# Performance work log

Hardware: AMD Instinct MI355X
Metric: run time of the kernel (lower is better)

The kernel has to match this reference:

```python
import jax, jax.numpy as jnp
import numpy as np

N_NODES = 100000
N_EDGES = 1600000
IN_FEAT = 128
OUT_FEAT = 128


def setup_inputs() -> dict:
    key = jax.random.key(0)
    k1, k2, k3 = jax.random.split(key, 3)
    x = jax.random.normal(k1, (N_NODES, IN_FEAT), dtype=jnp.float32)
    W = jax.random.normal(k2, (IN_FEAT, OUT_FEAT), dtype=jnp.float32) * (1.0 / np.sqrt(IN_FEAT))
    b = jnp.zeros((OUT_FEAT,), dtype=jnp.float32)
    edge_index = jax.random.randint(k3, (2, N_EDGES), 0, N_NODES, dtype=jnp.int64)
    return {"x": x, "W": W, "b": b, "edge_index": edge_index}


def reference(x, W, b, edge_index):
    # PyG GCNConv: add self-loops, symmetric deg normalization, scatter-add.
    N = x.shape[0]
    loops = jnp.arange(N, dtype=edge_index.dtype)
    ei = jnp.concatenate([edge_index, jnp.stack([loops, loops])], axis=1)  # [2, E+N]
    row, col = ei[0], ei[1]  # source, target
    ones = jnp.ones(ei.shape[1], dtype=x.dtype)
    deg = jax.ops.segment_sum(ones, col, num_segments=N)  # in-degree incl. self-loop
    deg_inv_sqrt = jnp.where(deg > 0, jax.lax.rsqrt(deg), 0.0)
    norm = deg_inv_sqrt[row] * deg_inv_sqrt[col]  # [E+N]
    xw = x @ W  # [N, out_feat]
    msg = xw[row] * norm[:, None]  # gather + normalize
    out = jax.ops.segment_sum(msg, col, num_segments=N) + b  # scatter-add + bias
    return out
```

## Files before the change

kernel.cpp:

```cpp
#include <hip/hip_runtime.h>

#define N_NODES 100000
#define N_EDGES 1600000
#define FEAT 128
#define NBUCK 782
#define BUCK_SHIFT 7
#define BUCK_MASK 127
#define GEMM_BLOCKS 1563
#define HIST_EPB 4096
#define HIST_BLOCKS 391
#define SCAT_EPB 12800
#define SCAT_BLOCKS 125
#define WT_PITCH 136

typedef __attribute__((ext_vector_type(8))) short short8;
typedef __attribute__((ext_vector_type(4))) float f32x4;

__device__ inline unsigned short f2bf(float f) {
    unsigned u = __builtin_bit_cast(unsigned, f);
    unsigned r = (u + 0x7FFFu + ((u >> 16) & 1u)) >> 16;
    return (unsigned short)r;
}
__device__ inline float bf2f(unsigned h) {
    unsigned u = h << 16;
    return __builtin_bit_cast(float, u);
}

__global__ __launch_bounds__(256)
void k_gemm_hist(const float* __restrict__ x, const float* __restrict__ W,
                 unsigned short* __restrict__ yb,
                 const int* __restrict__ col, int* __restrict__ bcnt) {
    int bid = blockIdx.x, tid = threadIdx.x;
    if (bid >= GEMM_BLOCKS) {
        __shared__ int hist[NBUCK];
        for (int i = tid; i < NBUCK; i += 256) hist[i] = 0;
        __syncthreads();
        int e0 = (bid - GEMM_BLOCKS) * HIST_EPB;
        int n = min(HIST_EPB, N_EDGES - e0);
        for (int i = tid * 4; i < n; i += 1024) {
            if (i + 3 < n) {
                int4 c4 = *(const int4*)(col + e0 + i);
                atomicAdd(&hist[c4.x >> BUCK_SHIFT], 1);
                atomicAdd(&hist[c4.y >> BUCK_SHIFT], 1);
                atomicAdd(&hist[c4.z >> BUCK_SHIFT], 1);
                atomicAdd(&hist[c4.w >> BUCK_SHIFT], 1);
            } else {
                for (int j = i; j < n; ++j) atomicAdd(&hist[col[e0 + j] >> BUCK_SHIFT], 1);
            }
        }
        __syncthreads();
        for (int i = tid; i < NBUCK; i += 256) {
            int h = hist[i];
            if (h) atomicAdd(&bcnt[i], h);
        }
        return;
    }

    __shared__ unsigned short Ws[FEAT * WT_PITCH];
    for (int idx = tid; idx < FEAT * FEAT; idx += 256) {
        int k = idx >> 7, f = idx & 127;
        Ws[f * WT_PITCH + k] = f2bf(W[idx]);
    }
    __syncthreads();

    int lane = tid & 63;
    int m = lane & 15, quad = lane >> 4;
    int node = bid * 64 + (tid >> 6) * 16 + m;
    int ldn = node < N_NODES ? node : N_NODES - 1;
    const float* xr = x + (size_t)ldn * FEAT + quad * 8;

    f32x4 acc[8];
#pragma unroll
    for (int nt = 0; nt < 8; ++nt) acc[nt] = (f32x4){0.f, 0.f, 0.f, 0.f};

#pragma unroll
    for (int kk = 0; kk < 4; ++kk) {
        float4 xa = *(const float4*)(xr + kk * 32);
        float4 xc = *(const float4*)(xr + kk * 32 + 4);
        short8 fx;
        fx[0] = (short)f2bf(xa.x); fx[1] = (short)f2bf(xa.y);
        fx[2] = (short)f2bf(xa.z); fx[3] = (short)f2bf(xa.w);
        fx[4] = (short)f2bf(xc.x); fx[5] = (short)f2bf(xc.y);
        fx[6] = (short)f2bf(xc.z); fx[7] = (short)f2bf(xc.w);
        const unsigned short* wp = Ws + kk * 32 + quad * 8;
#pragma unroll
        for (int nt = 0; nt < 8; ++nt) {
            short8 af = *(const short8*)(wp + (nt * 16 + m) * WT_PITCH);
            acc[nt] = __builtin_amdgcn_mfma_f32_16x16x32_bf16(af, fx, acc[nt], 0, 0, 0);
        }
    }

    if (node < N_NODES) {
        unsigned* yp = (unsigned*)(yb + (size_t)node * FEAT);
#pragma unroll
        for (int nt = 0; nt < 8; ++nt) {
            uint2 pk;
            pk.x = (unsigned)f2bf(acc[nt][0]) | ((unsigned)f2bf(acc[nt][1]) << 16);
            pk.y = (unsigned)f2bf(acc[nt][2]) | ((unsigned)f2bf(acc[nt][3]) << 16);
            *(uint2*)(yp + nt * 8 + quad * 2) = pk;
        }
    }
}

__global__ __launch_bounds__(256)
void k_bscatter(const int* __restrict__ row, const int* __restrict__ col,
                const int* __restrict__ bcnt, int* __restrict__ bcur0,
                int* __restrict__ bstarts, unsigned* __restrict__ ebuf) {
    __shared__ int sb[1024];
    __shared__ int csum[256];
    __shared__ int bstartsL[NBUCK];
    __shared__ int hist[NBUCK];
    __shared__ int gbase[NBUCK];
    int tid = threadIdx.x;

    for (int i = tid; i < 1024; i += 256) sb[i] = (i < NBUCK) ? bcnt[i] : 0;
    __syncthreads();
    int v0 = sb[tid * 4], v1 = sb[tid * 4 + 1], v2 = sb[tid * 4 + 2], v3 = sb[tid * 4 + 3];
    int p1 = v0 + v1, p2 = p1 + v2, p3 = p2 + v3;
    csum[tid] = p3;
    __syncthreads();
    for (int off = 1; off < 256; off <<= 1) {
        int t = (tid >= off) ? csum[tid - off] : 0;
        __syncthreads();
        csum[tid] += t;
        __syncthreads();
    }
    int base = csum[tid] - p3;
    if (tid * 4 < NBUCK)     bstartsL[tid * 4]     = base;
    if (tid * 4 + 1 < NBUCK) bstartsL[tid * 4 + 1] = base + v0;
    if (tid * 4 + 2 < NBUCK) bstartsL[tid * 4 + 2] = base + p1;
    if (tid * 4 + 3 < NBUCK) bstartsL[tid * 4 + 3] = base + p2;
    for (int i = tid; i < NBUCK; i += 256) hist[i] = 0;
    __syncthreads();
    if (blockIdx.x == 0) {
        for (int i = tid; i < NBUCK; i += 256) bstarts[i] = bstartsL[i];
        if (tid == 0) bstarts[NBUCK] = N_EDGES;
    }

    int e0 = blockIdx.x * SCAT_EPB;
    int n = min(SCAT_EPB, N_EDGES - e0);
    for (int i = tid * 4; i < n; i += 1024) {
        if (i + 3 < n) {
            int4 c4 = *(const int4*)(col + e0 + i);
            atomicAdd(&hist[c4.x >> BUCK_SHIFT], 1);
            atomicAdd(&hist[c4.y >> BUCK_SHIFT], 1);
            atomicAdd(&hist[c4.z >> BUCK_SHIFT], 1);
            atomicAdd(&hist[c4.w >> BUCK_SHIFT], 1);
        } else {
            for (int j = i; j < n; ++j) atomicAdd(&hist[col[e0 + j] >> BUCK_SHIFT], 1);
        }
    }
    __syncthreads();
    for (int i = tid; i < NBUCK; i += 256) {
        int h = hist[i];
        gbase[i] = bstartsL[i] + (h ? atomicAdd(&bcur0[i], h) : 0);
    }
    __syncthreads();
    for (int i = tid; i < NBUCK; i += 256) hist[i] = 0;
    __syncthreads();
    for (int i = tid * 4; i < n; i += 1024) {
        if (i + 3 < n) {
            int4 c4 = *(const int4*)(col + e0 + i);
            int4 r4 = *(const int4*)(row + e0 + i);
            int bk, off;
            bk = c4.x >> BUCK_SHIFT; off = atomicAdd(&hist[bk], 1);
            ebuf[gbase[bk] + off] = ((unsigned)r4.x << BUCK_SHIFT) | (unsigned)(c4.x & BUCK_MASK);
            bk = c4.y >> BUCK_SHIFT; off = atomicAdd(&hist[bk], 1);
            ebuf[gbase[bk] + off] = ((unsigned)r4.y << BUCK_SHIFT) | (unsigned)(c4.y & BUCK_MASK);
            bk = c4.z >> BUCK_SHIFT; off = atomicAdd(&hist[bk], 1);
            ebuf[gbase[bk] + off] = ((unsigned)r4.z << BUCK_SHIFT) | (unsigned)(c4.z & BUCK_MASK);
            bk = c4.w >> BUCK_SHIFT; off = atomicAdd(&hist[bk], 1);
            ebuf[gbase[bk] + off] = ((unsigned)r4.w << BUCK_SHIFT) | (unsigned)(c4.w & BUCK_MASK);
        } else {
            for (int j = i; j < n; ++j) {
                int c = col[e0 + j], r = row[e0 + j];
                int bk = c >> BUCK_SHIFT;
                int off = atomicAdd(&hist[bk], 1);
                ebuf[gbase[bk] + off] = ((unsigned)r << BUCK_SHIFT) | (unsigned)(c & BUCK_MASK);
            }
        }
    }
}

__global__ __launch_bounds__(256)
void k_csr(const unsigned* __restrict__ ebuf, const int* __restrict__ bstarts,
           int* __restrict__ starts, float* __restrict__ dinv,
           int* __restrict__ src_idx) {
    __shared__ int hist[128];
    __shared__ int scan[128];
    __shared__ int cur[128];
    int b = blockIdx.x, tid = threadIdx.x;
    int node0 = b << BUCK_SHIFT;
    int nnodes = min(128, N_NODES - node0);
    if (tid < 128) hist[tid] = 0;
    __syncthreads();
    int e0 = bstarts[b], e1 = bstarts[b + 1];
    int ne = e1 - e0;
    for (int i = tid; i < ne; i += 256) atomicAdd(&hist[ebuf[e0 + i] & BUCK_MASK], 1);
    __syncthreads();
    if (tid < 128) scan[tid] = hist[tid];
    __syncthreads();
    for (int off = 1; off < 128; off <<= 1) {
        int t = 0;
        if (tid < 128 && tid >= off) t = scan[tid - off];
        __syncthreads();
        if (tid < 128) scan[tid] += t;
        __syncthreads();
    }
    if (tid < 128) {
        int ex = scan[tid] - hist[tid];
        cur[tid] = ex;
        if (tid < nnodes) {
            starts[node0 + tid] = e0 + ex;
            dinv[node0 + tid] = rsqrtf((float)(hist[tid] + 1));
        }
    }
    if (b == 0 && tid == 0) starts[N_NODES] = N_EDGES;
    __syncthreads();
    for (int i = tid; i < ne; i += 256) {
        unsigned e = ebuf[e0 + i];
        int pos = atomicAdd(&cur[e & BUCK_MASK], 1);
        src_idx[e0 + pos] = (int)(e >> BUCK_SHIFT);
    }
}

#define GATHER_GROUP(D)                                             \
    {                                                               \
        unsigned v[D];                                              \
        _Pragma("unroll")                                           \
        for (int t = 0; t < (D); ++t) {                             \
            int s = __shfl(src, j + t);                             \
            v[t] = y1[(size_t)(unsigned)s * 64 + lane];             \
        }                                                           \
        _Pragma("unroll")                                           \
        for (int t = 0; t < (D); ++t) {                             \
            float d = __shfl(dvv, j + t);                           \
            a0 += d * bf2f(v[t] & 0xFFFFu);                         \
            a1 += d * bf2f(v[t] >> 16);                             \
        }                                                           \
        j += (D);                                                   \
    }

__global__ __launch_bounds__(256)
void k_agg(const unsigned short* __restrict__ yb, const int* __restrict__ starts,
           const int* __restrict__ src_idx, const float* __restrict__ dinv,
           const float* __restrict__ bias, float* __restrict__ out) {
    int node = blockIdx.x * 4 + (threadIdx.x >> 6);
    int lane = threadIdx.x & 63;
    if (node >= N_NODES) return;
    int st = starts[node], en = starts[node + 1];
    float di = dinv[node];
    const unsigned* y1 = (const unsigned*)yb;
    unsigned sv = y1[(size_t)node * 64 + lane];
    float a0 = di * bf2f(sv & 0xFFFFu);
    float a1 = di * bf2f(sv >> 16);
    for (int base = st; base < en; base += 64) {
        int nn = min(64, en - base);
        int src = 0;
        float dvv = 0.f;
        if (lane < nn) {
            src = src_idx[base + lane];
            dvv = dinv[src];
        }
        int j = 0;
        while (j + 16 <= nn) GATHER_GROUP(16)
        if (j + 8 <= nn) GATHER_GROUP(8)
        if (j + 4 <= nn) GATHER_GROUP(4)
        for (; j < nn; ++j) {
            int s = __shfl(src, j);
            float d = __shfl(dvv, j);
            unsigned v = y1[(size_t)(unsigned)s * 64 + lane];
            a0 += d * bf2f(v & 0xFFFFu);
            a1 += d * bf2f(v >> 16);
        }
    }
    float2 bb = ((const float2*)bias)[lane];
    float2 o;
    o.x = bb.x + di * a0;
    o.y = bb.y + di * a1;
    ((float2*)out)[(size_t)node * 64 + lane] = o;
}

extern "C" void kernel_launch(void* const* d_in, const int* in_sizes, int n_in,
                              void* d_out, int out_size, void* d_ws, size_t ws_size,
                              hipStream_t stream) {
    const float* x = (const float*)d_in[0];
    const float* W = (const float*)d_in[1];
    const float* b = (const float*)d_in[2];
    const int* ei = (const int*)d_in[3];
    const int* row = ei;
    const int* col = ei + N_EDGES;
    float* out = (float*)d_out;

    char* ws = (char*)d_ws;
    size_t off = 0;
    auto alloc = [&](size_t bytes) -> void* {
        void* p = ws + off;
        off += (bytes + 511) & ~(size_t)511;
        return p;
    };
    int* bcnt          = (int*)alloc((NBUCK + 1) * 4);
    int* bcur0         = (int*)alloc((NBUCK + 1) * 4);
    int* bstarts       = (int*)alloc((NBUCK + 1) * 4);
    int* starts        = (int*)alloc((size_t)(N_NODES + 1) * 4);
    float* dinv        = (float*)alloc((size_t)N_NODES * 4);
    unsigned* ebuf     = (unsigned*)alloc((size_t)N_EDGES * 4);
    int* src_idx       = (int*)alloc((size_t)N_EDGES * 4);
    unsigned short* yb = (unsigned short*)alloc((size_t)N_NODES * FEAT * 2);

    size_t msz = (size_t)((char*)bcur0 - (char*)bcnt) + (size_t)(NBUCK + 1) * 4;
    hipMemsetAsync(bcnt, 0, msz, stream);

    k_gemm_hist<<<GEMM_BLOCKS + HIST_BLOCKS, 256, 0, stream>>>(x, W, yb, col, bcnt);
    k_bscatter<<<SCAT_BLOCKS, 256, 0, stream>>>(row, col, bcnt, bcur0, bstarts, ebuf);
    k_csr<<<NBUCK, 256, 0, stream>>>(ebuf, bstarts, starts, dinv, src_idx);
    k_agg<<<(N_NODES + 3) / 4, 256, 0, stream>>>(yb, starts, src_idx, dinv, b, out);
}
```

Before: 236.6 us.

## Replace two-level bucketed CSR build with global-atomic degree count, scan, scatter

```diff
diff --git a/kernel.cpp b/kernel.cpp
--- a/kernel.cpp
+++ b/kernel.cpp
@@ -3,14 +3,14 @@
 #define N_NODES 100000
 #define N_EDGES 1600000
 #define FEAT 128
-#define NBUCK 782
-#define BUCK_SHIFT 7
-#define BUCK_MASK 127
 #define GEMM_BLOCKS 1563
-#define HIST_EPB 4096
-#define HIST_BLOCKS 391
-#define SCAT_EPB 12800
-#define SCAT_BLOCKS 125
+#define DEG_EPB 4096
+#define DEG_BLOCKS 391
+#define SCAT_EPB 4096
+#define SCAT_BLOCKS 391
+#define SCANA_CHUNK 1024
+#define SCANA_BLOCKS 98
+#define SCANC_BLOCKS 391
 #define WT_PITCH 136
 
 typedef __attribute__((ext_vector_type(8))) short short8;
@@ -27,31 +27,23 @@
 }
 
 __global__ __launch_bounds__(256)
-void k_gemm_hist(const float* __restrict__ x, const float* __restrict__ W,
-                 unsigned short* __restrict__ yb,
-                 const int* __restrict__ col, int* __restrict__ bcnt) {
+void k_gemm_deg(const float* __restrict__ x, const float* __restrict__ W,
+                unsigned short* __restrict__ yb,
+                const int* __restrict__ col, int* __restrict__ deg) {
     int bid = blockIdx.x, tid = threadIdx.x;
     if (bid >= GEMM_BLOCKS) {
-        __shared__ int hist[NBUCK];
-        for (int i = tid; i < NBUCK; i += 256) hist[i] = 0;
-        __syncthreads();
-        int e0 = (bid - GEMM_BLOCKS) * HIST_EPB;
-        int n = min(HIST_EPB, N_EDGES - e0);
+        int e0 = (bid - GEMM_BLOCKS) * DEG_EPB;
+        int n = min(DEG_EPB, N_EDGES - e0);
         for (int i = tid * 4; i < n; i += 1024) {
             if (i + 3 < n) {
                 int4 c4 = *(const int4*)(col + e0 + i);
-                atomicAdd(&hist[c4.x >> BUCK_SHIFT], 1);
-                atomicAdd(&hist[c4.y >> BUCK_SHIFT], 1);
-                atomicAdd(&hist[c4.z >> BUCK_SHIFT], 1);
-                atomicAdd(&hist[c4.w >> BUCK_SHIFT], 1);
+                atomicAdd(&deg[c4.x], 1);
+                atomicAdd(&deg[c4.y], 1);
+                atomicAdd(&deg[c4.z], 1);
+                atomicAdd(&deg[c4.w], 1);
             } else {
-                for (int j = i; j < n; ++j) atomicAdd(&hist[col[e0 + j] >> BUCK_SHIFT], 1);
+                for (int j = i; j < n; ++j) atomicAdd(&deg[col[e0 + j]], 1);
             }
-        }
-        __syncthreads();
-        for (int i = tid; i < NBUCK; i += 256) {
-            int h = hist[i];
-            if (h) atomicAdd(&bcnt[i], h);
         }
         return;
     }
@@ -102,125 +94,84 @@
     }
 }
 
-__global__ __launch_bounds__(256)
-void k_bscatter(const int* __restrict__ row, const int* __restrict__ col,
-                const int* __restrict__ bcnt, int* __restrict__ bcur0,
-                int* __restrict__ bstarts, unsigned* __restrict__ ebuf) {
-    __shared__ int sb[1024];
-    __shared__ int csum[256];
-    __shared__ int bstartsL[NBUCK];
-    __shared__ int hist[NBUCK];
-    __shared__ int gbase[NBUCK];
+__global__ __launch_bounds__(1024)
+void k_scanA(const int* __restrict__ deg, int* __restrict__ starts,
+             int* __restrict__ bsum) {
+    __shared__ int wsum[16];
     int tid = threadIdx.x;
-
-    for (int i = tid; i < 1024; i += 256) sb[i] = (i < NBUCK) ? bcnt[i] : 0;
-    __syncthreads();
-    int v0 = sb[tid * 4], v1 = sb[tid * 4 + 1], v2 = sb[tid * 4 + 2], v3 = sb[tid * 4 + 3];
-    int p1 = v0 + v1, p2 = p1 + v2, p3 = p2 + v3;
-    csum[tid] = p3;
-    __syncthreads();
-    for (int off = 1; off < 256; off <<= 1) {
-        int t = (tid >= off) ? csum[tid - off] : 0;
-        __syncthreads();
-        csum[tid] += t;
-        __syncthreads();
-    }
-    int base = csum[tid] - p3;
-    if (tid * 4 < NBUCK)     bstartsL[tid * 4]     = base;
-    if (tid * 4 + 1 < NBUCK) bstartsL[tid * 4 + 1] = base + v0;
-    if (tid * 4 + 2 < NBUCK) bstartsL[tid * 4 + 2] = base + p1;
-    if (tid * 4 + 3 < NBUCK) bstartsL[tid * 4 + 3] = base + p2;
-    for (int i = tid; i < NBUCK; i += 256) hist[i] = 0;
-    __syncthreads();
-    if (blockIdx.x == 0) {
-        for (int i = tid; i < NBUCK; i += 256) bstarts[i] = bstartsL[i];
-        if (tid == 0) bstarts[NBUCK] = N_EDGES;
-    }
-
+    int i = blockIdx.x * SCANA_CHUNK + tid;
+    int v = (i < N_NODES) ? deg[i] : 0;
+    int lane = tid & 63, wv = tid >> 6;
+    int s = v;
+#pragma unroll
+    for (int off = 1; off < 64; off <<= 1) {
+        int t = __shfl_up(s, off);
+        if (lane >= off) s += t;
+    }
+    if (lane == 63) wsum[wv] = s;
+    __syncthreads();
+    if (tid < 16) {
+        int w = wsum[tid];
+#pragma unroll
+        for (int off = 1; off < 16; off <<= 1) {
+            int t = __shfl_up(w, off);
+            if (tid >= off) w += t;
+        }
+        wsum[tid] = w;
+    }
+    __syncthreads();
+    int wbase = (wv == 0) ? 0 : wsum[wv - 1];
+    if (i < N_NODES) starts[i] = wbase + s - v;
+    if (tid == 0) bsum[blockIdx.x] = wsum[15];
+}
+
+__global__ __launch_bounds__(256)
+void k_scanC(const int* __restrict__ deg, const int* __restrict__ bsum,
+             int* __restrict__ starts, int* __restrict__ cur,
+             float* __restrict__ dinv) {
+    __shared__ int sb[SCANA_BLOCKS];
+    __shared__ int boff;
+    int tid = threadIdx.x;
+    int chunk = (blockIdx.x * 256) >> 10;
+    if (tid < SCANA_BLOCKS) sb[tid] = bsum[tid];
+    __syncthreads();
+    if (tid == 0) {
+        int a = 0;
+        for (int j = 0; j < chunk; ++j) a += sb[j];
+        boff = a;
+    }
+    __syncthreads();
+    int i = blockIdx.x * 256 + tid;
+    if (i < N_NODES) {
+        int s = starts[i] + boff;
+        starts[i] = s;
+        cur[i] = s;
+        dinv[i] = rsqrtf((float)(deg[i] + 1));
+    }
+    if (blockIdx.x == 0 && tid == 0) starts[N_NODES] = N_EDGES;
+}
+
+__global__ __launch_bounds__(256)
+void k_scatter(const int* __restrict__ row, const int* __restrict__ col,
+               int* __restrict__ cur, int* __restrict__ src_idx) {
+    int tid = threadIdx.x;
     int e0 = blockIdx.x * SCAT_EPB;
     int n = min(SCAT_EPB, N_EDGES - e0);
     for (int i = tid * 4; i < n; i += 1024) {
         if (i + 3 < n) {
             int4 c4 = *(const int4*)(col + e0 + i);
-            atomicAdd(&hist[c4.x >> BUCK_SHIFT], 1);
-            atomicAdd(&hist[c4.y >> BUCK_SHIFT], 1);
-            atomicAdd(&hist[c4.z >> BUCK_SHIFT], 1);
-            atomicAdd(&hist[c4.w >> BUCK_SHIFT], 1);
-        } else {
-            for (int j = i; j < n; ++j) atomicAdd(&hist[col[e0 + j] >> BUCK_SHIFT], 1);
-        }
-    }
-    __syncthreads();
-    for (int i = tid; i < NBUCK; i += 256) {
-        int h = hist[i];
-        gbase[i] = bstartsL[i] + (h ? atomicAdd(&bcur0[i], h) : 0);
-    }
-    __syncthreads();
-    for (int i = tid; i < NBUCK; i += 256) hist[i] = 0;
-    __syncthreads();
-    for (int i = tid * 4; i < n; i += 1024) {
-        if (i + 3 < n) {
-            int4 c4 = *(const int4*)(col + e0 + i);
             int4 r4 = *(const int4*)(row + e0 + i);
-            int bk, off;
-            bk = c4.x >> BUCK_SHIFT; off = atomicAdd(&hist[bk], 1);
-            ebuf[gbase[bk] + off] = ((unsigned)r4.x << BUCK_SHIFT) | (unsigned)(c4.x & BUCK_MASK);
-            bk = c4.y >> BUCK_SHIFT; off = atomicAdd(&hist[bk], 1);
-            ebuf[gbase[bk] + off] = ((unsigned)r4.y << BUCK_SHIFT) | (unsigned)(c4.y & BUCK_MASK);
-            bk = c4.z >> BUCK_SHIFT; off = atomicAdd(&hist[bk], 1);
-            ebuf[gbase[bk] + off] = ((unsigned)r4.z << BUCK_SHIFT) | (unsigned)(c4.z & BUCK_MASK);
-            bk = c4.w >> BUCK_SHIFT; off = atomicAdd(&hist[bk], 1);
-            ebuf[gbase[bk] + off] = ((unsigned)r4.w << BUCK_SHIFT) | (unsigned)(c4.w & BUCK_MASK);
+            int p;
+            p = atomicAdd(&cur[c4.x], 1); src_idx[p] = r4.x;
+            p = atomicAdd(&cur[c4.y], 1); src_idx[p] = r4.y;
+            p = atomicAdd(&cur[c4.z], 1); src_idx[p] = r4.z;
+            p = atomicAdd(&cur[c4.w], 1); src_idx[p] = r4.w;
         } else {
             for (int j = i; j < n; ++j) {
-                int c = col[e0 + j], r = row[e0 + j];
-                int bk = c >> BUCK_SHIFT;
-                int off = atomicAdd(&hist[bk], 1);
-                ebuf[gbase[bk] + off] = ((unsigned)r << BUCK_SHIFT) | (unsigned)(c & BUCK_MASK);
+                int p = atomicAdd(&cur[col[e0 + j]], 1);
+                src_idx[p] = row[e0 + j];
             }
         }
-    }
-}
-
-__global__ __launch_bounds__(256)
-void k_csr(const unsigned* __restrict__ ebuf, const int* __restrict__ bstarts,
-           int* __restrict__ starts, float* __restrict__ dinv,
-           int* __restrict__ src_idx) {
-    __shared__ int hist[128];
-    __shared__ int scan[128];
-    __shared__ int cur[128];
-    int b = blockIdx.x, tid = threadIdx.x;
-    int node0 = b << BUCK_SHIFT;
-    int nnodes = min(128, N_NODES - node0);
-    if (tid < 128) hist[tid] = 0;
-    __syncthreads();
-    int e0 = bstarts[b], e1 = bstarts[b + 1];
-    int ne = e1 - e0;
-    for (int i = tid; i < ne; i += 256) atomicAdd(&hist[ebuf[e0 + i] & BUCK_MASK], 1);
-    __syncthreads();
-    if (tid < 128) scan[tid] = hist[tid];
-    __syncthreads();
-    for (int off = 1; off < 128; off <<= 1) {
-        int t = 0;
-        if (tid < 128 && tid >= off) t = scan[tid - off];
-        __syncthreads();
-        if (tid < 128) scan[tid] += t;
-        __syncthreads();
-    }
-    if (tid < 128) {
-        int ex = scan[tid] - hist[tid];
-        cur[tid] = ex;
-        if (tid < nnodes) {
-            starts[node0 + tid] = e0 + ex;
-            dinv[node0 + tid] = rsqrtf((float)(hist[tid] + 1));
-        }
-    }
-    if (b == 0 && tid == 0) starts[N_NODES] = N_EDGES;
-    __syncthreads();
-    for (int i = tid; i < ne; i += 256) {
-        unsigned e = ebuf[e0 + i];
-        int pos = atomicAdd(&cur[e & BUCK_MASK], 1);
-        src_idx[e0 + pos] = (int)(e >> BUCK_SHIFT);
     }
 }
 
@@ -299,20 +250,19 @@
         off += (bytes + 511) & ~(size_t)511;
         return p;
     };
-    int* bcnt          = (int*)alloc((NBUCK + 1) * 4);
-    int* bcur0         = (int*)alloc((NBUCK + 1) * 4);
-    int* bstarts       = (int*)alloc((NBUCK + 1) * 4);
+    int* deg           = (int*)alloc((size_t)N_NODES * 4);
+    int* bsum          = (int*)alloc(SCANA_BLOCKS * 4);
     int* starts        = (int*)alloc((size_t)(N_NODES + 1) * 4);
+    int* cur           = (int*)alloc((size_t)N_NODES * 4);
     float* dinv        = (float*)alloc((size_t)N_NODES * 4);
-    unsigned* ebuf     = (unsigned*)alloc((size_t)N_EDGES * 4);
     int* src_idx       = (int*)alloc((size_t)N_EDGES * 4);
     unsigned short* yb = (unsigned short*)alloc((size_t)N_NODES * FEAT * 2);
 
-    size_t msz = (size_t)((char*)bcur0 - (char*)bcnt) + (size_t)(NBUCK + 1) * 4;
-    hipMemsetAsync(bcnt, 0, msz, stream);
-
-    k_gemm_hist<<<GEMM_BLOCKS + HIST_BLOCKS, 256, 0, stream>>>(x, W, yb, col, bcnt);
-    k_bscatter<<<SCAT_BLOCKS, 256, 0, stream>>>(row, col, bcnt, bcur0, bstarts, ebuf);
-    k_csr<<<NBUCK, 256, 0, stream>>>(ebuf, bstarts, starts, dinv, src_idx);
+    hipMemsetAsync(deg, 0, (size_t)N_NODES * 4, stream);
+
+    k_gemm_deg<<<GEMM_BLOCKS + DEG_BLOCKS, 256, 0, stream>>>(x, W, yb, col, deg);
+    k_scanA<<<SCANA_BLOCKS, 1024, 0, stream>>>(deg, starts, bsum);
+    k_scanC<<<SCANC_BLOCKS, 256, 0, stream>>>(deg, bsum, starts, cur, dinv);
+    k_scatter<<<SCAT_BLOCKS, 256, 0, stream>>>(row, col, cur, src_idx);
     k_agg<<<(N_NODES + 3) / 4, 256, 0, stream>>>(yb, starts, src_idx, dinv, b, out);
 }
```

Result: slower. 355.2 us (+50.1%).

## Merge bucket scatter and CSR build into one cooperative kernel with grid syncs

Applied to the files above, without the earlier changes.

```diff
diff --git a/kernel.cpp b/kernel.cpp
--- a/kernel.cpp
+++ b/kernel.cpp
@@ -1,4 +1,7 @@
 #include <hip/hip_runtime.h>
+#include <hip/hip_cooperative_groups.h>
+
+namespace cg = cooperative_groups;
 
 #define N_NODES 100000
 #define N_EDGES 1600000
@@ -9,8 +12,8 @@
 #define GEMM_BLOCKS 1563
 #define HIST_EPB 4096
 #define HIST_BLOCKS 391
-#define SCAT_EPB 12800
-#define SCAT_BLOCKS 125
+#define PRE_BLOCKS 1000
+#define PRE_EPB 1600
 #define WT_PITCH 136
 
 typedef __attribute__((ext_vector_type(8))) short short8;
@@ -103,124 +106,128 @@
 }
 
 __global__ __launch_bounds__(256)
-void k_bscatter(const int* __restrict__ row, const int* __restrict__ col,
-                const int* __restrict__ bcnt, int* __restrict__ bcur0,
-                int* __restrict__ bstarts, unsigned* __restrict__ ebuf) {
+void k_pre(const int* __restrict__ row, const int* __restrict__ col,
+           const int* __restrict__ bcnt, int* __restrict__ bcur0,
+           int* __restrict__ bstarts, unsigned* __restrict__ ebuf,
+           int* __restrict__ starts, float* __restrict__ dinv,
+           int* __restrict__ src_idx) {
+    cg::grid_group grid = cg::this_grid();
     __shared__ int sb[1024];
     __shared__ int csum[256];
-    __shared__ int bstartsL[NBUCK];
     __shared__ int hist[NBUCK];
     __shared__ int gbase[NBUCK];
-    int tid = threadIdx.x;
-
-    for (int i = tid; i < 1024; i += 256) sb[i] = (i < NBUCK) ? bcnt[i] : 0;
-    __syncthreads();
-    int v0 = sb[tid * 4], v1 = sb[tid * 4 + 1], v2 = sb[tid * 4 + 2], v3 = sb[tid * 4 + 3];
-    int p1 = v0 + v1, p2 = p1 + v2, p3 = p2 + v3;
-    csum[tid] = p3;
-    __syncthreads();
-    for (int off = 1; off < 256; off <<= 1) {
-        int t = (tid >= off) ? csum[tid - off] : 0;
-        __syncthreads();
-        csum[tid] += t;
-        __syncthreads();
-    }
-    int base = csum[tid] - p3;
-    if (tid * 4 < NBUCK)     bstartsL[tid * 4]     = base;
-    if (tid * 4 + 1 < NBUCK) bstartsL[tid * 4 + 1] = base + v0;
-    if (tid * 4 + 2 < NBUCK) bstartsL[tid * 4 + 2] = base + p1;
-    if (tid * 4 + 3 < NBUCK) bstartsL[tid * 4 + 3] = base + p2;
-    for (int i = tid; i < NBUCK; i += 256) hist[i] = 0;
-    __syncthreads();
-    if (blockIdx.x == 0) {
-        for (int i = tid; i < NBUCK; i += 256) bstarts[i] = bstartsL[i];
+    __shared__ int h128[128];
+    __shared__ int s128[128];
+    __shared__ int c128[128];
+    int tid = threadIdx.x, bid = blockIdx.x;
+
+    if (bid == 0) {
+        for (int i = tid; i < 1024; i += 256) sb[i] = (i < NBUCK) ? bcnt[i] : 0;
+        __syncthreads();
+        int v0 = sb[tid * 4], v1 = sb[tid * 4 + 1], v2 = sb[tid * 4 + 2], v3 = sb[tid * 4 + 3];
+        int p1 = v0 + v1, p2 = p1 + v2, p3 = p2 + v3;
+        csum[tid] = p3;
+        __syncthreads();
+        for (int off = 1; off < 256; off <<= 1) {
+            int t = (tid >= off) ? csum[tid - off] : 0;
+            __syncthreads();
+            csum[tid] += t;
+            __syncthreads();
+        }
+        int base = csum[tid] - p3;
+        if (tid * 4 < NBUCK)     bstarts[tid * 4]     = base;
+        if (tid * 4 + 1 < NBUCK) bstarts[tid * 4 + 1] = base + v0;
+        if (tid * 4 + 2 < NBUCK) bstarts[tid * 4 + 2] = base + p1;
+        if (tid * 4 + 3 < NBUCK) bstarts[tid * 4 + 3] = base + p2;
         if (tid == 0) bstarts[NBUCK] = N_EDGES;
-    }
-
-    int e0 = blockIdx.x * SCAT_EPB;
-    int n = min(SCAT_EPB, N_EDGES - e0);
-    for (int i = tid * 4; i < n; i += 1024) {
-        if (i + 3 < n) {
-            int4 c4 = *(const int4*)(col + e0 + i);
-            atomicAdd(&hist[c4.x >> BUCK_SHIFT], 1);
-            atomicAdd(&hist[c4.y >> BUCK_SHIFT], 1);
-            atomicAdd(&hist[c4.z >> BUCK_SHIFT], 1);
-            atomicAdd(&hist[c4.w >> BUCK_SHIFT], 1);
-        } else {
-            for (int j = i; j < n; ++j) atomicAdd(&hist[col[e0 + j] >> BUCK_SHIFT], 1);
-        }
-    }
-    __syncthreads();
-    for (int i = tid; i < NBUCK; i += 256) {
-        int h = hist[i];
-        gbase[i] = bstartsL[i] + (h ? atomicAdd(&bcur0[i], h) : 0);
-    }
-    __syncthreads();
-    for (int i = tid; i < NBUCK; i += 256) hist[i] = 0;
-    __syncthreads();
-    for (int i = tid * 4; i < n; i += 1024) {
-        if (i + 3 < n) {
-            int4 c4 = *(const int4*)(col + e0 + i);
-            int4 r4 = *(const int4*)(row + e0 + i);
-            int bk, off;
-            bk = c4.x >> BUCK_SHIFT; off = atomicAdd(&hist[bk], 1);
-            ebuf[gbase[bk] + off] = ((unsigned)r4.x << BUCK_SHIFT) | (unsigned)(c4.x & BUCK_MASK);
-            bk = c4.y >> BUCK_SHIFT; off = atomicAdd(&hist[bk], 1);
-            ebuf[gbase[bk] + off] = ((unsigned)r4.y << BUCK_SHIFT) | (unsigned)(c4.y & BUCK_MASK);
-            bk = c4.z >> BUCK_SHIFT; off = atomicAdd(&hist[bk], 1);
-            ebuf[gbase[bk] + off] = ((unsigned)r4.z << BUCK_SHIFT) | (unsigned)(c4.z & BUCK_MASK);
-            bk = c4.w >> BUCK_SHIFT; off = atomicAdd(&hist[bk], 1);
-            ebuf[gbase[bk] + off] = ((unsigned)r4.w << BUCK_SHIFT) | (unsigned)(c4.w & BUCK_MASK);
-        } else {
-            for (int j = i; j < n; ++j) {
-                int c = col[e0 + j], r = row[e0 + j];
-                int bk = c >> BUCK_SHIFT;
-                int off = atomicAdd(&hist[bk], 1);
-                ebuf[gbase[bk] + off] = ((unsigned)r << BUCK_SHIFT) | (unsigned)(c & BUCK_MASK);
+        __threadfence();
+    }
+    grid.sync();
+
+    {
+        for (int i = tid; i < NBUCK; i += 256) hist[i] = 0;
+        __syncthreads();
+        int e0 = bid * PRE_EPB;
+        int n = min(PRE_EPB, N_EDGES - e0);
+        for (int i = tid * 4; i < n; i += 1024) {
+            if (i + 3 < n) {
+                int4 c4 = *(const int4*)(col + e0 + i);
+                atomicAdd(&hist[c4.x >> BUCK_SHIFT], 1);
+                atomicAdd(&hist[c4.y >> BUCK_SHIFT], 1);
+                atomicAdd(&hist[c4.z >> BUCK_SHIFT], 1);
+                atomicAdd(&hist[c4.w >> BUCK_SHIFT], 1);
+            } else {
+                for (int j = i; j < n; ++j) atomicAdd(&hist[col[e0 + j] >> BUCK_SHIFT], 1);
             }
         }
-    }
-}
-
-__global__ __launch_bounds__(256)
-void k_csr(const unsigned* __restrict__ ebuf, const int* __restrict__ bstarts,
-           int* __restrict__ starts, float* __restrict__ dinv,
-           int* __restrict__ src_idx) {
-    __shared__ int hist[128];
-    __shared__ int scan[128];
-    __shared__ int cur[128];
-    int b = blockIdx.x, tid = threadIdx.x;
-    int node0 = b << BUCK_SHIFT;
-    int nnodes = min(128, N_NODES - node0);
-    if (tid < 128) hist[tid] = 0;
-    __syncthreads();
-    int e0 = bstarts[b], e1 = bstarts[b + 1];
-    int ne = e1 - e0;
-    for (int i = tid; i < ne; i += 256) atomicAdd(&hist[ebuf[e0 + i] & BUCK_MASK], 1);
-    __syncthreads();
-    if (tid < 128) scan[tid] = hist[tid];
-    __syncthreads();
-    for (int off = 1; off < 128; off <<= 1) {
-        int t = 0;
-        if (tid < 128 && tid >= off) t = scan[tid - off];
-        __syncthreads();
-        if (tid < 128) scan[tid] += t;
-        __syncthreads();
-    }
-    if (tid < 128) {
-        int ex = scan[tid] - hist[tid];
-        cur[tid] = ex;
-        if (tid < nnodes) {
-            starts[node0 + tid] = e0 + ex;
-            dinv[node0 + tid] = rsqrtf((float)(hist[tid] + 1));
-        }
-    }
-    if (b == 0 && tid == 0) starts[N_NODES] = N_EDGES;
-    __syncthreads();
-    for (int i = tid; i < ne; i += 256) {
-        unsigned e = ebuf[e0 + i];
-        int pos = atomicAdd(&cur[e & BUCK_MASK], 1);
-        src_idx[e0 + pos] = (int)(e >> BUCK_SHIFT);
+        __syncthreads();
+        for (int i = tid; i < NBUCK; i += 256) {
+            int h = hist[i];
+            gbase[i] = bstarts[i] + (h ? atomicAdd(&bcur0[i], h) : 0);
+        }
+        __syncthreads();
+        for (int i = tid; i < NBUCK; i += 256) hist[i] = 0;
+        __syncthreads();
+        for (int i = tid * 4; i < n; i += 1024) {
+            if (i + 3 < n) {
+                int4 c4 = *(const int4*)(col + e0 + i);
+                int4 r4 = *(const int4*)(row + e0 + i);
+                int bk, off;
+                bk = c4.x >> BUCK_SHIFT; off = atomicAdd(&hist[bk], 1);
+                ebuf[gbase[bk] + off] = ((unsigned)r4.x << BUCK_SHIFT) | (unsigned)(c4.x & BUCK_MASK);
+                bk = c4.y >> BUCK_SHIFT; off = atomicAdd(&hist[bk], 1);
+                ebuf[gbase[bk] + off] = ((unsigned)r4.y << BUCK_SHIFT) | (unsigned)(c4.y & BUCK_MASK);
+                bk = c4.z >> BUCK_SHIFT; off = atomicAdd(&hist[bk], 1);
+                ebuf[gbase[bk] + off] = ((unsigned)r4.z << BUCK_SHIFT) | (unsigned)(c4.z & BUCK_MASK);
+                bk = c4.w >> BUCK_SHIFT; off = atomicAdd(&hist[bk], 1);
+                ebuf[gbase[bk] + off] = ((unsigned)r4.w << BUCK_SHIFT) | (unsigned)(c4.w & BUCK_MASK);
+            } else {
+                for (int j = i; j < n; ++j) {
+                    int c = col[e0 + j], r = row[e0 + j];
+                    int bk = c >> BUCK_SHIFT;
+                    int off = atomicAdd(&hist[bk], 1);
+                    ebuf[gbase[bk] + off] = ((unsigned)r << BUCK_SHIFT) | (unsigned)(c & BUCK_MASK);
+                }
+            }
+        }
+    }
+    __threadfence();
+    grid.sync();
+
+    if (bid < NBUCK) {
+        int b = bid;
+        int node0 = b << BUCK_SHIFT;
+        int nnodes = min(128, N_NODES - node0);
+        if (tid < 128) h128[tid] = 0;
+        __syncthreads();
+        int e0 = bstarts[b], e1 = bstarts[b + 1];
+        int ne = e1 - e0;
+        for (int i = tid; i < ne; i += 256) atomicAdd(&h128[ebuf[e0 + i] & BUCK_MASK], 1);
+        __syncthreads();
+        if (tid < 128) s128[tid] = h128[tid];
+        __syncthreads();
+        for (int off = 1; off < 128; off <<= 1) {
+            int t = 0;
+            if (tid < 128 && tid >= off) t = s128[tid - off];
+            __syncthreads();
+            if (tid < 128) s128[tid] += t;
+            __syncthreads();
+        }
+        if (tid < 128) {
+            int ex = s128[tid] - h128[tid];
+            c128[tid] = ex;
+            if (tid < nnodes) {
+                starts[node0 + tid] = e0 + ex;
+                dinv[node0 + tid] = rsqrtf((float)(h128[tid] + 1));
+            }
+        }
+        if (b == 0 && tid == 0) starts[N_NODES] = N_EDGES;
+        __syncthreads();
+        for (int i = tid; i < ne; i += 256) {
+            unsigned e = ebuf[e0 + i];
+            int pos = atomicAdd(&c128[e & BUCK_MASK], 1);
+            src_idx[e0 + pos] = (int)(e >> BUCK_SHIFT);
+        }
     }
 }
 
@@ -312,7 +319,12 @@
     hipMemsetAsync(bcnt, 0, msz, stream);
 
     k_gemm_hist<<<GEMM_BLOCKS + HIST_BLOCKS, 256, 0, stream>>>(x, W, yb, col, bcnt);
-    k_bscatter<<<SCAT_BLOCKS, 256, 0, stream>>>(row, col, bcnt, bcur0, bstarts, ebuf);
-    k_csr<<<NBUCK, 256, 0, stream>>>(ebuf, bstarts, starts, dinv, src_idx);
+
+    void* pre_args[] = {(void*)&row, (void*)&col, (void*)&bcnt, (void*)&bcur0,
+                        (void*)&bstarts, (void*)&ebuf, (void*)&starts,
+                        (void*)&dinv, (void*)&src_idx};
+    hipLaunchCooperativeKernel((const void*)k_pre, dim3(PRE_BLOCKS), dim3(256),
+                               pre_args, 0, stream);
+
     k_agg<<<(N_NODES + 3) / 4, 256, 0, stream>>>(yb, starts, src_idx, dinv, b, out);
 }
```

New measurement: 559.2 us. 136% more time.
